# Kernel tuning notes

Measured on AMD Instinct MI355X. Metric: run time of the kernel, lower is better.

## Reference

```python
import jax, jax.numpy as jnp
import numpy as np
import math

H = 8
D_MODEL = 32
D_HEAD = 4
FACTOR = 5
EPS = 1e-5

DATANUM = 1024
B = 512            # outer batch; becomes attention sequence length
C = 32
L = DATANUM // 8   # 128; becomes attention batch
U = min(FACTOR * int(math.ceil(math.log(B))), B)  # 35 (U_part == u since L_Q == L_K == B)


def setup_inputs() -> dict:
    key = jax.random.key(0)
    ks = jax.random.split(key, 16)
    s = 0.05
    return {
        'x': jax.random.normal(ks[0], (B, C, L), jnp.float32),
        'Wq': jax.random.normal(ks[1], (D_MODEL, D_MODEL), jnp.float32) * s,
        'bq': jnp.zeros((D_MODEL,), jnp.float32),
        'Wk': jax.random.normal(ks[2], (D_MODEL, D_MODEL), jnp.float32) * s,
        'bk': jnp.zeros((D_MODEL,), jnp.float32),
        'Wv': jax.random.normal(ks[3], (D_MODEL, D_MODEL), jnp.float32) * s,
        'bv': jnp.zeros((D_MODEL,), jnp.float32),
        'Wo': jax.random.normal(ks[4], (D_MODEL, D_MODEL), jnp.float32) * s,
        'bo': jnp.zeros((D_MODEL,), jnp.float32),
        'bn1_gamma': jnp.ones((C,), jnp.float32),
        'bn1_beta': jnp.zeros((C,), jnp.float32),
        'bn1_mean': jnp.zeros((C,), jnp.float32),
        'bn1_var': jnp.ones((C,), jnp.float32),
        'W1': jax.random.normal(ks[5], (DATANUM * 8, DATANUM * 4), jnp.float32) * 0.01,
        'b1': jnp.zeros((DATANUM * 8,), jnp.float32),
        'W2': jax.random.normal(ks[6], (DATANUM * 4, DATANUM * 8), jnp.float32) * 0.01,
        'b2': jnp.zeros((DATANUM * 4,), jnp.float32),
        'bn2_gamma': jnp.ones((C,), jnp.float32),
        'bn2_beta': jnp.zeros((C,), jnp.float32),
        'bn2_mean': jnp.zeros((C,), jnp.float32),
        'bn2_var': jnp.ones((C,), jnp.float32),
        'index_sample': jax.random.randint(ks[7], (B, U), 0, B, jnp.int64),
    }


def _bn(x, gamma, beta, mean, var):
    # eval-mode BatchNorm1d over channel dim of (batch, C, length)
    inv = jax.lax.rsqrt(var + EPS)
    return (x - mean[None, :, None]) * (inv * gamma)[None, :, None] + beta[None, :, None]


def _prob_attention(Q, K, V, index_sample):
    # Q,K,V: (Ba, H, Lq, D) self-attention, Lq == Lk. Informer ProbAttention, mask_flag=True.
    Ba, Hh, Lq, D = Q.shape
    u = index_sample.shape[1]
    # sparsity measurement on sampled keys
    K_sample = K[:, :, index_sample, :]                       # (Ba,H,Lq,U,D)
    QK_sample = jnp.einsum('bhld,bhlud->bhlu', Q, K_sample)
    M = QK_sample.max(axis=-1) - QK_sample.sum(axis=-1) / Lq  # (Ba,H,Lq)
    _, M_top = jax.lax.top_k(M, u)                            # (Ba,H,u) selected queries
    Q_reduce = jnp.take_along_axis(Q, M_top[..., None], axis=2)  # (Ba,H,u,D)
    scores = jnp.einsum('bhud,bhkd->bhuk', Q_reduce, K) / jnp.sqrt(jnp.float32(D))
    # ProbMask: causal w.r.t. the selected query's original position
    causal = jnp.arange(Lq)[None, None, None, :] > M_top[..., None]
    scores = jnp.where(causal, -jnp.inf, scores)
    attn = jax.nn.softmax(scores, axis=-1)
    upd = jnp.einsum('bhuk,bhkd->bhud', attn, V)              # (Ba,H,u,D)
    context = jnp.cumsum(V, axis=2)                           # initial context (mask_flag=True)
    b_idx = jnp.arange(Ba)[:, None, None]
    h_idx = jnp.arange(Hh)[None, :, None]
    context = context.at[b_idx, h_idx, M_top].set(upd)
    return context


def reference(x, Wq, bq, Wk, bk, Wv, bv, Wo, bo,
              bn1_gamma, bn1_beta, bn1_mean, bn1_var,
              W1, b1, W2, b2,
              bn2_gamma, bn2_beta, bn2_mean, bn2_var,
              index_sample):
    Bsz, Cc, Ll = x.shape
    res1 = x
    xa = jnp.transpose(x, (2, 0, 1))                          # (L, B, 32): attn batch=L, seq=B

    def heads(t):
        return jnp.transpose(t.reshape(Ll, Bsz, H, D_HEAD), (0, 2, 1, 3))

    Q = heads(xa @ Wq.T + bq)
    K = heads(xa @ Wk.T + bk)
    V = heads(xa @ Wv.T + bv)
    ctx = _prob_attention(Q, K, V, index_sample)              # (L,H,B,D)
    out = jnp.transpose(ctx, (0, 2, 1, 3)).reshape(Ll, Bsz, D_MODEL)
    out = out @ Wo.T + bo
    xh = jax.nn.relu(out)                                     # dropout = identity (eval)
    xh = jnp.transpose(xh, (1, 2, 0))                         # (B,32,L)
    xh = _bn(xh + res1, bn1_gamma, bn1_beta, bn1_mean, bn1_var)
    res2 = xh
    f = xh.reshape(Bsz, Cc * Ll)
    f = jax.nn.relu(f @ W1.T + b1)
    f = jax.nn.relu(f @ W2.T + b2)
    f = f.reshape(Bsz, Cc, Ll)
    return _bn(f + res2, bn2_gamma, bn2_beta, bn2_mean, bn2_var)
```

## Files before the change

### kernel.cpp

```cpp
#include <hip/hip_runtime.h>
#include <stdint.h>

#define EPSF 1e-5f
#define NEG_INF (-1e30f)

typedef float f32x4 __attribute__((ext_vector_type(4)));
typedef __bf16 bf16x8 __attribute__((ext_vector_type(8)));
typedef unsigned short u16x8 __attribute__((ext_vector_type(8)));

typedef __attribute__((address_space(3))) unsigned char* as3_ptr;
typedef const __attribute__((address_space(1))) unsigned char* as1_ptr;

__device__ __forceinline__ void async16(const void* g, void* l) {
  __builtin_amdgcn_global_load_lds((as1_ptr)g, (as3_ptr)l, 16, 0, 0);
}

__device__ __forceinline__ unsigned short f2bf(float f) {
  union { float f; unsigned int u; } v; v.f = f;
  unsigned int r = v.u + 0x7FFFu + ((v.u >> 16) & 1u);
  return (unsigned short)(r >> 16);
}
__device__ __forceinline__ unsigned short f2bf_fast(float f) {
  union { float f; unsigned int u; } v; v.f = f;
  return (unsigned short)((v.u + 0x8000u) >> 16);
}

__global__ __launch_bounds__(256) void transpose_k(const float* __restrict__ src,
                                                   float* __restrict__ dst, int R, int C) {
  __shared__ float tl[32][33];
  int tx = threadIdx.x & 31, ty = threadIdx.x >> 5;
  int c0 = blockIdx.x * 32, r0 = blockIdx.y * 32;
#pragma unroll
  for (int i = 0; i < 4; i++)
    tl[ty + i * 8][tx] = src[(size_t)(r0 + ty + i * 8) * C + c0 + tx];
  __syncthreads();
#pragma unroll
  for (int i = 0; i < 4; i++)
    dst[(size_t)(c0 + ty + i * 8) * R + r0 + tx] = tl[tx][ty + i * 8];
}

__global__ __launch_bounds__(256) void qkv_k(const float* __restrict__ xT,
    const float* __restrict__ Wq, const float* __restrict__ bq,
    const float* __restrict__ Wk, const float* __restrict__ bk,
    const float* __restrict__ Wv, const float* __restrict__ bv,
    float* __restrict__ Q, float* __restrict__ Kq, float* __restrict__ Vq) {
  __shared__ float xs[64 * 33];
  __shared__ float wq[32 * 33], wk[32 * 33], wvs[32 * 33];
  __shared__ float bqs[32], bks[32], bvs[32];
  int tid = threadIdx.x;
  int a = blockIdx.x;
  int tbase = blockIdx.y * 256;
#pragma unroll
  for (int i = 0; i < 4; i++) {
    int e = i * 256 + tid; int r = e >> 5, c = e & 31;
    wq[r * 33 + c] = Wq[e]; wk[r * 33 + c] = Wk[e]; wvs[r * 33 + c] = Wv[e];
  }
  if (tid < 32) { bqs[tid] = bq[tid]; bks[tid] = bk[tid]; bvs[tid] = bv[tid]; }
  int tl = tid & 63, rg = tid >> 6;
  for (int ch = 0; ch < 4; ch++) {
    __syncthreads();
#pragma unroll
    for (int i = 0; i < 8; i++) {
      int e = i * 256 + tid; int r = e >> 5, c = e & 31;
      xs[r * 33 + c] = xT[(size_t)a * 16384 + (size_t)(tbase + ch * 64) * 32 + e];
    }
    __syncthreads();
    float qa[8], ka[8], va[8];
#pragma unroll
    for (int r8 = 0; r8 < 8; r8++) {
      int r = rg * 8 + r8; qa[r8] = bqs[r]; ka[r8] = bks[r]; va[r8] = bvs[r];
    }
    for (int c = 0; c < 32; c++) {
      float xv = xs[tl * 33 + c];
#pragma unroll
      for (int r8 = 0; r8 < 8; r8++) {
        int r = rg * 8 + r8;
        qa[r8] += xv * wq[r * 33 + c];
        ka[r8] += xv * wk[r * 33 + c];
        va[r8] += xv * wvs[r * 33 + c];
      }
    }
    int t = tbase + ch * 64 + tl;
#pragma unroll
    for (int r8 = 0; r8 < 8; r8++) {
      int r = rg * 8 + r8;
      size_t o = (size_t)a * 16384 + (size_t)r * 512 + t;
      Q[o] = qa[r8]; Kq[o] = ka[r8]; Vq[o] = va[r8];
    }
  }
}

__global__ __launch_bounds__(512) void topattn_k(const float* __restrict__ Q,
    const float* __restrict__ Kq, const float* __restrict__ Vq,
    const int* __restrict__ idxs, float* __restrict__ Ctx, int U) {
  __shared__ float Ks[2048];
  __shared__ float Vs[2048];
  __shared__ float Ml[512];
  __shared__ int mt[64];
  __shared__ float Qr[64][4];
  __shared__ float upd[64][4];
  int bh = blockIdx.x;
  int tid = threadIdx.x, lane = tid & 63, wv = tid >> 6;
  size_t base = (size_t)bh * 2048;
#pragma unroll
  for (int i = 0; i < 4; i++) {
    Ks[i * 512 + tid] = Kq[base + i * 512 + tid];
    Vs[i * 512 + tid] = Vq[base + i * 512 + tid];
  }
  float q0 = Q[base + tid], q1 = Q[base + 512 + tid];
  float q2 = Q[base + 1024 + tid], q3 = Q[base + 1536 + tid];
  __syncthreads();
  float mx = NEG_INF, sm = 0.f;
  for (int u = 0; u < U; u++) {
    int it = idxs[tid * U + u];
    it = min(max(it, 0), 511);
    float s = q0 * Ks[it] + q1 * Ks[512 + it] + q2 * Ks[1024 + it] + q3 * Ks[1536 + it];
    mx = fmaxf(mx, s); sm += s;
  }
  Ml[tid] = mx - sm * (1.f / 512.f);
  __syncthreads();
  float mi = Ml[tid];
  int rank = 0;
  for (int j0 = 0; j0 < 512; j0 += 4) {
    float4 m4 = *(const float4*)(Ml + j0);
    rank += (m4.x > mi) || (m4.x == mi && (j0 + 0) < tid);
    rank += (m4.y > mi) || (m4.y == mi && (j0 + 1) < tid);
    rank += (m4.z > mi) || (m4.z == mi && (j0 + 2) < tid);
    rank += (m4.w > mi) || (m4.w == mi && (j0 + 3) < tid);
  }
  if (rank < U) mt[rank] = tid;
  __syncthreads();
  if (tid < 4 * U) { int u = tid >> 2, d = tid & 3; Qr[u][d] = Q[base + d * 512 + mt[u]]; }
  __syncthreads();
  for (int u = wv; u < U; u += 8) {
    int mrow = mt[u];
    float p0q = Qr[u][0], p1q = Qr[u][1], p2q = Qr[u][2], p3q = Qr[u][3];
    float sv[8]; float lmax = NEG_INF;
#pragma unroll
    for (int jj = 0; jj < 8; jj++) {
      int k = jj * 64 + lane;
      float s = NEG_INF;
      if (k <= mrow)
        s = 0.5f * (p0q * Ks[k] + p1q * Ks[512 + k] + p2q * Ks[1024 + k] + p3q * Ks[1536 + k]);
      sv[jj] = s; lmax = fmaxf(lmax, s);
    }
#pragma unroll
    for (int off = 32; off; off >>= 1) lmax = fmaxf(lmax, __shfl_xor(lmax, off));
    float ls = 0.f, p0 = 0.f, p1 = 0.f, p2 = 0.f, p3 = 0.f;
#pragma unroll
    for (int jj = 0; jj < 8; jj++) {
      int k = jj * 64 + lane;
      if (k <= mrow) {
        float p = __expf(sv[jj] - lmax);
        ls += p; p0 += p * Vs[k]; p1 += p * Vs[512 + k];
        p2 += p * Vs[1024 + k]; p3 += p * Vs[1536 + k];
      }
    }
#pragma unroll
    for (int off = 32; off; off >>= 1) {
      ls += __shfl_xor(ls, off); p0 += __shfl_xor(p0, off); p1 += __shfl_xor(p1, off);
      p2 += __shfl_xor(p2, off); p3 += __shfl_xor(p3, off);
    }
    if (lane == 0) {
      float inv = 1.f / ls;
      upd[u][0] = p0 * inv; upd[u][1] = p1 * inv; upd[u][2] = p2 * inv; upd[u][3] = p3 * inv;
    }
  }
  __syncthreads();
  if (wv < 4) {
    float v[8];
    int b0 = wv * 512 + lane * 8;
#pragma unroll
    for (int q = 0; q < 8; q++) v[q] = Vs[b0 + q];
#pragma unroll
    for (int q = 1; q < 8; q++) v[q] += v[q - 1];
    float x = v[7];
    for (int off = 1; off < 64; off <<= 1) {
      float y = __shfl_up(x, off);
      if (lane >= off) x += y;
    }
    float excl = x - v[7];
#pragma unroll
    for (int q = 0; q < 8; q++) Vs[b0 + q] = v[q] + excl;
  }
  __syncthreads();
  if (tid < 4 * U) { int u = tid >> 2, d = tid & 3; Vs[d * 512 + mt[u]] = upd[u][d]; }
  __syncthreads();
#pragma unroll
  for (int i = 0; i < 4; i++) Ctx[base + i * 512 + tid] = Vs[i * 512 + tid];
}

__global__ __launch_bounds__(256) void oproj_k(const float* __restrict__ Ctx,
    const float* __restrict__ Wo, const float* __restrict__ bo, float* __restrict__ Y) {
  __shared__ float cs[32 * 256];
  __shared__ float wo[32 * 33];
  __shared__ float bos[32];
  int tid = threadIdx.x;
  int a = blockIdx.x, t0 = blockIdx.y * 256;
#pragma unroll
  for (int i = 0; i < 4; i++) {
    int e = i * 256 + tid; int r = e >> 5, c = e & 31;
    wo[r * 33 + c] = Wo[e];
  }
  if (tid < 32) bos[tid] = bo[tid];
#pragma unroll
  for (int i = 0; i < 32; i++) {
    int e = i * 256 + tid; int row = e >> 8, col = e & 255;
    cs[e] = Ctx[(size_t)a * 16384 + (size_t)row * 512 + t0 + col];
  }
  __syncthreads();
  int rl = tid & 31, tw = tid >> 5;
  for (int ti = 0; ti < 32; ti++) {
    int t = ti * 8 + tw;
    float acc = bos[rl];
#pragma unroll
    for (int rp = 0; rp < 32; rp++) acc += cs[rp * 256 + t] * wo[rl * 33 + rp];
    Y[(size_t)a * 16384 + (size_t)(t0 + t) * 32 + rl] = acc;
  }
}

__global__ __launch_bounds__(256) void bn1t_k(const float* __restrict__ Y,
    const float* __restrict__ x, const float* __restrict__ g1, const float* __restrict__ be1,
    const float* __restrict__ me1, const float* __restrict__ va1,
    float* __restrict__ Xh, unsigned short* __restrict__ Fb) {
  __shared__ float tl[32][33];
  int tx = threadIdx.x & 31, ty = threadIdx.x >> 5;
  int c0 = blockIdx.x * 32;
  int r0 = blockIdx.y * 32;
#pragma unroll
  for (int i = 0; i < 4; i++)
    tl[ty + i * 8][tx] = Y[(size_t)(r0 + ty + i * 8) * 16384 + c0 + tx];
  __syncthreads();
#pragma unroll
  for (int i = 0; i < 4; i++) {
    int m = c0 + ty + i * 8;
    int a = r0 + tx;
    float v = tl[tx][ty + i * 8];
    int ch = m & 31;
    size_t oi = (size_t)m * 128 + a;
    float val = fmaxf(v, 0.f) + x[oi];
    float s = g1[ch] * rsqrtf(va1[ch] + EPSF);
    float res = (val - me1[ch]) * s + be1[ch];
    Xh[oi] = res;
    Fb[oi] = f2bf(res);
  }
}

__global__ __launch_bounds__(256, 3) void gemm_fb(
    const unsigned short* __restrict__ A, const float* __restrict__ Bw,
    int K, int N, int MT, int NPX, int SPLITK, float* __restrict__ P, int M) {
  __shared__ unsigned char lds[8192 + 16384];
  int tid = threadIdx.x;
  int lane = tid & 63, wv = tid >> 6;
  int wm = wv >> 1, wn = wv & 1;
  int lin = blockIdx.x;
  int xcd = lin & 7, slot = lin >> 3;
  int tilesPerSp = MT * NPX;
  int sp = slot / tilesPerSp;
  int rem = slot % tilesPerSp;
  int mt = rem % MT;
  int nt = xcd * NPX + rem / MT;
  int mtile0 = mt * 128, ntile0 = nt * 128;
  int m0 = mtile0 + wm * 64, n0 = ntile0 + wn * 64;
  int frow = lane & 15, q = lane >> 4;

  int nk = K / (32 * SPLITK);
  int kbase = sp * (K / SPLITK);

  f32x4 acc[4][4];
#pragma unroll
  for (int i = 0; i < 4; i++)
#pragma unroll
    for (int j = 0; j < 4; j++) { f32x4 z = {0.f, 0.f, 0.f, 0.f}; acc[i][j] = z; }

  for (int k = 0; k < nk; k++) {
    int ks = kbase + k * 32;
#pragma unroll
    for (int i = 0; i < 2; i++) {
      int e = i * 256 + tid;
      int row = e >> 2;
      int g = (e & 3) ^ ((row >> 1) & 3);
      async16(A + (size_t)(mtile0 + row) * K + ks + g * 8, lds + i * 4096 + wv * 1024);
    }
#pragma unroll
    for (int i = 0; i < 4; i++) {
      int e = i * 256 + tid;
      int row = e >> 3;
      int g = (e & 7) ^ (row & 7);
      async16(Bw + (size_t)(ntile0 + row) * K + ks + g * 4,
              lds + 8192 + i * 4096 + wv * 1024);
    }
    __syncthreads();
    bf16x8 af[4], bfr[4];
#pragma unroll
    for (int i = 0; i < 4; i++) {
      int row = wm * 64 + i * 16 + frow;
      af[i] = *(const bf16x8*)(lds + row * 64 + ((q ^ ((row >> 1) & 3)) << 4));
    }
#pragma unroll
    for (int j = 0; j < 4; j++) {
      int row = wn * 64 + j * 16 + frow;
      const unsigned char* rb = lds + 8192 + row * 128;
      int sw = row & 7;
      float4 w0 = *(const float4*)(rb + (((2 * q + 0) ^ sw) << 4));
      float4 w1 = *(const float4*)(rb + (((2 * q + 1) ^ sw) << 4));
      bf16x8 b;
      b[0] = (__bf16)w0.x; b[1] = (__bf16)w0.y; b[2] = (__bf16)w0.z; b[3] = (__bf16)w0.w;
      b[4] = (__bf16)w1.x; b[5] = (__bf16)w1.y; b[6] = (__bf16)w1.z; b[7] = (__bf16)w1.w;
      bfr[j] = b;
    }
#pragma unroll
    for (int i = 0; i < 4; i++)
#pragma unroll
      for (int j = 0; j < 4; j++)
        acc[i][j] = __builtin_amdgcn_mfma_f32_16x16x32_bf16(af[i], bfr[j], acc[i][j], 0, 0, 0);
    __syncthreads();
  }

  float* pb = P + (size_t)sp * M * N;
#pragma unroll
  for (int i = 0; i < 4; i++)
#pragma unroll
    for (int j = 0; j < 4; j++) {
      int n = n0 + j * 16 + frow;
      int mb = m0 + i * 16 + (q << 2);
#pragma unroll
      for (int r = 0; r < 4; r++)
        pb[(size_t)(mb + r) * N + n] = acc[i][j][r];
    }
}

template <int MI, int NJ, int EPI>
__global__ __launch_bounds__(256) void gemm_ps(
    const unsigned short* __restrict__ A, const float* __restrict__ Bw,
    const float* __restrict__ bias, int K, int N, int MT, int NPX, int SPLITK,
    float* __restrict__ Pout, int M,
    unsigned short* __restrict__ Hout, const float* __restrict__ res2,
    const float* __restrict__ g2, const float* __restrict__ be2,
    const float* __restrict__ me2, const float* __restrict__ va2,
    float* __restrict__ Out) {
  constexpr int BM = MI * 32;
  constexpr int BN = NJ * 32;
  constexpr int ABYTES = BM * 32 * 2;
  constexpr int BBYTES = BN * 32 * 4;
  constexpr int SA = ABYTES / 4096;
  constexpr int SB = BBYTES / 4096;
  __shared__ unsigned char lds[ABYTES + BBYTES];
  int tid = threadIdx.x;
  int lane = tid & 63, wv = tid >> 6;
  int wm = wv >> 1, wn = wv & 1;
  int lin = blockIdx.x;
  int xcd = lin & 7, slot = lin >> 3;
  int tilesPerSp = MT * NPX;
  int sp = slot / tilesPerSp;
  int rem = slot % tilesPerSp;
  int mt = rem % MT;
  int nt = xcd * NPX + rem / MT;
  int m0 = mt * BM + wm * (BM / 2);
  int n0 = nt * BN + wn * (BN / 2);
  int frow = lane & 15, q = lane >> 4;
  int nk = K / (32 * SPLITK);
  int kbase = sp * (K / SPLITK);
  f32x4 acc[MI][NJ];
#pragma unroll
  for (int i = 0; i < MI; i++)
#pragma unroll
    for (int j = 0; j < NJ; j++) { f32x4 z = {0.f, 0.f, 0.f, 0.f}; acc[i][j] = z; }
  int mtile0 = mt * BM, ntile0 = nt * BN;
  for (int k = 0; k < nk; k++) {
    int ks = kbase + k * 32;
#pragma unroll
    for (int i = 0; i < SA; i++) {
      int e = i * 256 + tid;
      int row = e >> 2;
      int g = (e & 3) ^ ((row >> 1) & 3);
      async16(A + (size_t)(mtile0 + row) * K + ks + g * 8, lds + i * 4096 + wv * 1024);
    }
#pragma unroll
    for (int i = 0; i < SB; i++) {
      int e = i * 256 + tid;
      int row = e >> 3;
      int g = (e & 7) ^ (row & 7);
      async16(Bw + (size_t)(ntile0 + row) * K + ks + g * 4,
              lds + ABYTES + i * 4096 + wv * 1024);
    }
    __syncthreads();
    bf16x8 af[MI];
    bf16x8 bfr[NJ];
#pragma unroll
    for (int i = 0; i < MI; i++) {
      int row = wm * (BM / 2) + i * 16 + frow;
      af[i] = *(const bf16x8*)(lds + row * 64 + ((q ^ ((row >> 1) & 3)) << 4));
    }
#pragma unroll
    for (int j = 0; j < NJ; j++) {
      int row = wn * (BN / 2) + j * 16 + frow;
      const unsigned char* rb = lds + ABYTES + row * 128;
      int sw = row & 7;
      float4 w0 = *(const float4*)(rb + (((2 * q + 0) ^ sw) << 4));
      float4 w1 = *(const float4*)(rb + (((2 * q + 1) ^ sw) << 4));
      union { u16x8 u; bf16x8 b; } cv;
      cv.u[0] = f2bf_fast(w0.x); cv.u[1] = f2bf_fast(w0.y);
      cv.u[2] = f2bf_fast(w0.z); cv.u[3] = f2bf_fast(w0.w);
      cv.u[4] = f2bf_fast(w1.x); cv.u[5] = f2bf_fast(w1.y);
      cv.u[6] = f2bf_fast(w1.z); cv.u[7] = f2bf_fast(w1.w);
      bfr[j] = cv.b;
    }
#pragma unroll
    for (int i = 0; i < MI; i++)
#pragma unroll
      for (int j = 0; j < NJ; j++)
        acc[i][j] = __builtin_amdgcn_mfma_f32_16x16x32_bf16(af[i], bfr[j], acc[i][j], 0, 0, 0);
    __syncthreads();
  }
#pragma unroll
  for (int i = 0; i < MI; i++)
#pragma unroll
    for (int j = 0; j < NJ; j++) {
      int n = n0 + j * 16 + frow;
      int mb = m0 + i * 16 + (q << 2);
      if constexpr (EPI == 2) {
        float* pb = Pout + (size_t)sp * M * N;
#pragma unroll
        for (int r = 0; r < 4; r++)
          pb[(size_t)(mb + r) * N + n] = acc[i][j][r];
      } else if constexpr (EPI == 0) {
        float bb = bias[n];
#pragma unroll
        for (int r = 0; r < 4; r++) {
          float v = fmaxf(acc[i][j][r] + bb, 0.f);
          Hout[(size_t)(mb + r) * N + n] = f2bf(v);
        }
      } else {
        float bb = bias[n];
        int ch = n >> 7;
        float s = g2[ch] * rsqrtf(va2[ch] + EPSF);
        float mu = me2[ch], bt = be2[ch];
#pragma unroll
        for (int r = 0; r < 4; r++) {
          float v = fmaxf(acc[i][j][r] + bb, 0.f);
          size_t oi = (size_t)(mb + r) * N + n;
          v += res2[oi];
          Out[oi] = (v - mu) * s + bt;
        }
      }
    }
}

template <int EPI>
__global__ __launch_bounds__(256) void red_k(const float* __restrict__ P, int SP,
    const float* __restrict__ bias, const float* __restrict__ Xh,
    const float* __restrict__ g2, const float* __restrict__ be2,
    const float* __restrict__ me2, const float* __restrict__ va2,
    unsigned short* __restrict__ H, float* __restrict__ Out, int N, int MN) {
  int idx = blockIdx.x * 256 + threadIdx.x;
  const float4* p = (const float4*)P;
  int mn4 = MN >> 2;
  float4 s = p[idx];
  for (int sp = 1; sp < SP; sp++) {
    float4 t = p[idx + (size_t)sp * mn4];
    s.x += t.x; s.y += t.y; s.z += t.z; s.w += t.w;
  }
  int n = (idx << 2) & (N - 1);
  float4 bb = *(const float4*)(bias + n);
  if constexpr (EPI == 0) {
    ushort4 o;
    o.x = f2bf(fmaxf(s.x + bb.x, 0.f));
    o.y = f2bf(fmaxf(s.y + bb.y, 0.f));
    o.z = f2bf(fmaxf(s.z + bb.z, 0.f));
    o.w = f2bf(fmaxf(s.w + bb.w, 0.f));
    ((ushort4*)H)[idx] = o;
  } else {
    int ch = n >> 7;
    float sc = g2[ch] * rsqrtf(va2[ch] + EPSF);
    float mu = me2[ch], bt = be2[ch];
    float4 xh = ((const float4*)Xh)[idx];
    float4 o;
    o.x = (fmaxf(s.x + bb.x, 0.f) + xh.x - mu) * sc + bt;
    o.y = (fmaxf(s.y + bb.y, 0.f) + xh.y - mu) * sc + bt;
    o.z = (fmaxf(s.z + bb.z, 0.f) + xh.z - mu) * sc + bt;
    o.w = (fmaxf(s.w + bb.w, 0.f) + xh.w - mu) * sc + bt;
    ((float4*)Out)[idx] = o;
  }
}

extern "C" void kernel_launch(void* const* d_in, const int* in_sizes, int n_in,
                              void* d_out, int out_size, void* d_ws, size_t ws_size,
                              hipStream_t stream) {
  const float* x  = (const float*)d_in[0];
  const float* Wq = (const float*)d_in[1];  const float* bq = (const float*)d_in[2];
  const float* Wk = (const float*)d_in[3];  const float* bk = (const float*)d_in[4];
  const float* Wv = (const float*)d_in[5];  const float* bv = (const float*)d_in[6];
  const float* Wo = (const float*)d_in[7];  const float* bo = (const float*)d_in[8];
  const float* g1 = (const float*)d_in[9];  const float* be1 = (const float*)d_in[10];
  const float* me1 = (const float*)d_in[11]; const float* va1 = (const float*)d_in[12];
  const float* W1 = (const float*)d_in[13]; const float* b1 = (const float*)d_in[14];
  const float* W2 = (const float*)d_in[15]; const float* b2 = (const float*)d_in[16];
  const float* g2 = (const float*)d_in[17]; const float* be2 = (const float*)d_in[18];
  const float* me2 = (const float*)d_in[19]; const float* va2 = (const float*)d_in[20];
  const int* idxs = (const int*)d_in[21];
  int U = in_sizes[21] / 512;
  float* out = (float*)d_out;

  char* ws = (char*)d_ws;
  float* QC = (float*)(ws);
  float* Kb = (float*)(ws + (8u << 20));
  float* Vb = (float*)(ws + (16u << 20));
  float* YT = (float*)(ws + (24u << 20));
  float* Xh = (float*)(ws + (32u << 20));
  unsigned short* Fb = (unsigned short*)Vb;
  unsigned short* Hb = (unsigned short*)Kb;
  float* PA = (float*)(ws + (48u << 20));
  bool main_tier = ws_size >= (size_t)84 * (1u << 20);

  dim3 b256(256);
  transpose_k<<<dim3(4, 512), b256, 0, stream>>>(x, YT, 16384, 128);
  qkv_k<<<dim3(128, 2), b256, 0, stream>>>(YT, Wq, bq, Wk, bk, Wv, bv, QC, Kb, Vb);
  topattn_k<<<dim3(1024), dim3(512), 0, stream>>>(QC, Kb, Vb, idxs, QC, U);
  oproj_k<<<dim3(128, 2), b256, 0, stream>>>(QC, Wo, bo, YT);
  bn1t_k<<<dim3(512, 4), b256, 0, stream>>>(YT, x, g1, be1, me1, va1, Xh, Fb);

  if (main_tier) {
    gemm_fb<<<dim3(512), b256, 0, stream>>>(Fb, W1, 4096, 8192, 4, 8, 2, PA, 512);
    red_k<0><<<dim3(4096), b256, 0, stream>>>(PA, 2, b1, nullptr, nullptr, nullptr,
                                              nullptr, nullptr, Hb, nullptr, 8192,
                                              512 * 8192);
    gemm_fb<<<dim3(512), b256, 0, stream>>>(Hb, W2, 8192, 4096, 4, 4, 4, PA, 512);
    red_k<1><<<dim3(2048), b256, 0, stream>>>(PA, 4, b2, Xh, g2, be2, me2, va2,
                                              nullptr, out, 4096, 512 * 4096);
  } else {
    gemm_ps<4, 2, 0><<<dim3(512), b256, 0, stream>>>(
        Fb, W1, b1, 4096, 8192, 4, 16, 1, nullptr, 512,
        Hb, nullptr, nullptr, nullptr, nullptr, nullptr, nullptr);
    gemm_ps<4, 2, 1><<<dim3(256), b256, 0, stream>>>(
        Hb, W2, b2, 8192, 4096, 4, 8, 1, nullptr, 512,
        nullptr, Xh, g2, be2, me2, va2, out);
  }
}
```

Baseline: 562.3 us.

## Convert fp32 weights to bf16 before LDS store and double split-K

The GEMM kernel now loads fp32 weight tiles into registers, converts them to bf16, and stores them to LDS. Before, it copied raw fp32 tiles asynchronously and converted them on every fragment read. This halves the weight LDS footprint, which allows four blocks per CU, and removes repeated conversion work. Split-K is doubled for both GEMMs, giving twice the blocks at the cost of larger partial buffers and more reduction traffic. Because of that, the workspace threshold is raised, and the loss of asynchronous weight loads may expose more global latency.

```diff
diff --git a/kernel.cpp b/kernel.cpp
--- a/kernel.cpp
+++ b/kernel.cpp
@@ -246,10 +246,10 @@
   }
 }
 
-__global__ __launch_bounds__(256, 3) void gemm_fb(
+__global__ __launch_bounds__(256, 4) void gemm_fb2(
     const unsigned short* __restrict__ A, const float* __restrict__ Bw,
     int K, int N, int MT, int NPX, int SPLITK, float* __restrict__ P, int M) {
-  __shared__ unsigned char lds[8192 + 16384];
+  __shared__ unsigned char lds[16384];
   int tid = threadIdx.x;
   int lane = tid & 63, wv = tid >> 6;
   int wm = wv >> 1, wn = wv & 1;
@@ -267,6 +267,13 @@
   int nk = K / (32 * SPLITK);
   int kbase = sp * (K / SPLITK);
 
+  int brow = tid >> 1;
+  int g0 = (tid & 1) * 2;
+  const float* bsrc = Bw + (size_t)(ntile0 + brow) * K + kbase + g0 * 8;
+  int bsw = (brow >> 1) & 3;
+  unsigned char* bdst0 = lds + 8192 + brow * 64 + (((g0 + 0) ^ bsw) << 4);
+  unsigned char* bdst1 = lds + 8192 + brow * 64 + (((g0 + 1) ^ bsw) << 4);
+
   f32x4 acc[4][4];
 #pragma unroll
   for (int i = 0; i < 4; i++)
@@ -275,6 +282,8 @@
 
   for (int k = 0; k < nk; k++) {
     int ks = kbase + k * 32;
+    const float4* bp = (const float4*)(bsrc + (size_t)k * 32);
+    float4 bv0 = bp[0], bv1 = bp[1], bv2 = bp[2], bv3 = bp[3];
 #pragma unroll
     for (int i = 0; i < 2; i++) {
       int e = i * 256 + tid;
@@ -282,14 +291,13 @@
       int g = (e & 3) ^ ((row >> 1) & 3);
       async16(A + (size_t)(mtile0 + row) * K + ks + g * 8, lds + i * 4096 + wv * 1024);
     }
-#pragma unroll
-    for (int i = 0; i < 4; i++) {
-      int e = i * 256 + tid;
-      int row = e >> 3;
-      int g = (e & 7) ^ (row & 7);
-      async16(Bw + (size_t)(ntile0 + row) * K + ks + g * 4,
-              lds + 8192 + i * 4096 + wv * 1024);
-    }
+    bf16x8 w0, w1;
+    w0[0] = (__bf16)bv0.x; w0[1] = (__bf16)bv0.y; w0[2] = (__bf16)bv0.z; w0[3] = (__bf16)bv0.w;
+    w0[4] = (__bf16)bv1.x; w0[5] = (__bf16)bv1.y; w0[6] = (__bf16)bv1.z; w0[7] = (__bf16)bv1.w;
+    w1[0] = (__bf16)bv2.x; w1[1] = (__bf16)bv2.y; w1[2] = (__bf16)bv2.z; w1[3] = (__bf16)bv2.w;
+    w1[4] = (__bf16)bv3.x; w1[5] = (__bf16)bv3.y; w1[6] = (__bf16)bv3.z; w1[7] = (__bf16)bv3.w;
+    *(bf16x8*)bdst0 = w0;
+    *(bf16x8*)bdst1 = w1;
     __syncthreads();
     bf16x8 af[4], bfr[4];
 #pragma unroll
@@ -300,14 +308,7 @@
 #pragma unroll
     for (int j = 0; j < 4; j++) {
       int row = wn * 64 + j * 16 + frow;
-      const unsigned char* rb = lds + 8192 + row * 128;
-      int sw = row & 7;
-      float4 w0 = *(const float4*)(rb + (((2 * q + 0) ^ sw) << 4));
-      float4 w1 = *(const float4*)(rb + (((2 * q + 1) ^ sw) << 4));
-      bf16x8 b;
-      b[0] = (__bf16)w0.x; b[1] = (__bf16)w0.y; b[2] = (__bf16)w0.z; b[3] = (__bf16)w0.w;
-      b[4] = (__bf16)w1.x; b[5] = (__bf16)w1.y; b[6] = (__bf16)w1.z; b[7] = (__bf16)w1.w;
-      bfr[j] = b;
+      bfr[j] = *(const bf16x8*)(lds + 8192 + row * 64 + ((q ^ ((row >> 1) & 3)) << 4));
     }
 #pragma unroll
     for (int i = 0; i < 4; i++)
@@ -511,7 +512,7 @@
   unsigned short* Fb = (unsigned short*)Vb;
   unsigned short* Hb = (unsigned short*)Kb;
   float* PA = (float*)(ws + (48u << 20));
-  bool main_tier = ws_size >= (size_t)84 * (1u << 20);
+  bool main_tier = ws_size >= (size_t)120 * (1u << 20);
 
   dim3 b256(256);
   transpose_k<<<dim3(4, 512), b256, 0, stream>>>(x, YT, 16384, 128);
@@ -521,12 +522,12 @@
   bn1t_k<<<dim3(512, 4), b256, 0, stream>>>(YT, x, g1, be1, me1, va1, Xh, Fb);
 
   if (main_tier) {
-    gemm_fb<<<dim3(512), b256, 0, stream>>>(Fb, W1, 4096, 8192, 4, 8, 2, PA, 512);
-    red_k<0><<<dim3(4096), b256, 0, stream>>>(PA, 2, b1, nullptr, nullptr, nullptr,
+    gemm_fb2<<<dim3(1024), b256, 0, stream>>>(Fb, W1, 4096, 8192, 4, 8, 4, PA, 512);
+    red_k<0><<<dim3(4096), b256, 0, stream>>>(PA, 4, b1, nullptr, nullptr, nullptr,
                                               nullptr, nullptr, Hb, nullptr, 8192,
                                               512 * 8192);
-    gemm_fb<<<dim3(512), b256, 0, stream>>>(Hb, W2, 8192, 4096, 4, 4, 4, PA, 512);
-    red_k<1><<<dim3(2048), b256, 0, stream>>>(PA, 4, b2, Xh, g2, be2, me2, va2,
+    gemm_fb2<<<dim3(1024), b256, 0, stream>>>(Hb, W2, 8192, 4096, 4, 4, 8, PA, 512);
+    red_k<1><<<dim3(2048), b256, 0, stream>>>(PA, 8, b2, Xh, g2, be2, me2, va2,
                                               nullptr, out, 4096, 512 * 4096);
   } else {
     gemm_ps<4, 2, 0><<<dim3(512), b256, 0, stream>>>(
```

Result: no change. 571.2 us (+1.6%).
